# Kernel optimization log

Hardware: AMD Instinct MI355X
Metric: run time of the kernel (lower is better)

## Reference

```python
import jax, jax.numpy as jnp
import numpy as np

D = 512      # units / model dim
H = 8        # num_heads
K = 512      # key_dim (= units in this module)
B = 8
T = 512      # decoder length
S = 512      # encoder length
EPS = 1e-3   # Keras LayerNormalization default epsilon


def _layernorm(x, g, b):
    mu = jnp.mean(x, axis=-1, keepdims=True)
    var = jnp.mean(jnp.square(x - mu), axis=-1, keepdims=True)
    return (x - mu) * jax.lax.rsqrt(var + EPS) * g + b


def _mha(q_in, kv_in, wq, bq, wk, bk, wv, bv, wo, bo, causal):
    # q_in: [B,Tq,D], kv_in: [B,Tk,D]; wq/wk/wv: [D,H,K]; wo: [H,K,D]
    q = jnp.einsum('btd,dhk->bthk', q_in, wq) + bq
    k = jnp.einsum('bsd,dhk->bshk', kv_in, wk) + bk
    v = jnp.einsum('bsd,dhk->bshk', kv_in, wv) + bv
    scores = jnp.einsum('bqhk,bshk->bhqs', q, k) / jnp.sqrt(jnp.float32(K))
    if causal:
        Tq, Tk = q.shape[1], k.shape[1]
        mask = jnp.tril(jnp.ones((Tq, Tk), dtype=bool))
        scores = jnp.where(mask[None, None], scores, jnp.finfo(scores.dtype).min)
    attn = jax.nn.softmax(scores, axis=-1)
    out = jnp.einsum('bhqs,bshk->bqhk', attn, v)
    return jnp.einsum('bqhk,hkd->bqd', out, wo) + bo


def setup_inputs() -> dict:
    key = jax.random.key(0)
    ks = jax.random.split(key, 32)
    sc = 0.02
    d = {
        'in_seq': jax.random.normal(ks[0], (B, S, D), jnp.float32),
        'out_seq': jax.random.normal(ks[1], (B, T, D), jnp.float32),
    }
    i = 2
    for pfx in ('sa', 'ca'):
        d[pfx + '_wq'] = jax.random.normal(ks[i], (D, H, K)) * sc; i += 1
        d[pfx + '_bq'] = jnp.zeros((H, K))
        d[pfx + '_wk'] = jax.random.normal(ks[i], (D, H, K)) * sc; i += 1
        d[pfx + '_bk'] = jnp.zeros((H, K))
        d[pfx + '_wv'] = jax.random.normal(ks[i], (D, H, K)) * sc; i += 1
        d[pfx + '_bv'] = jnp.zeros((H, K))
        d[pfx + '_wo'] = jax.random.normal(ks[i], (H, K, D)) * sc; i += 1
        d[pfx + '_bo'] = jnp.zeros((D,))
        d[pfx + '_lng'] = jnp.ones((D,))
        d[pfx + '_lnb'] = jnp.zeros((D,))
    d['ff_w1'] = jax.random.normal(ks[i], (D, 2 * D)) * sc; i += 1
    d['ff_b1'] = jnp.zeros((2 * D,))
    d['ff_w2'] = jax.random.normal(ks[i], (2 * D, D)) * sc; i += 1
    d['ff_b2'] = jnp.zeros((D,))
    d['ff_lng'] = jnp.ones((D,))
    d['ff_lnb'] = jnp.zeros((D,))
    return d


def reference(in_seq, out_seq,
              sa_wq, sa_bq, sa_wk, sa_bk, sa_wv, sa_bv, sa_wo, sa_bo, sa_lng, sa_lnb,
              ca_wq, ca_bq, ca_wk, ca_bk, ca_wv, ca_bv, ca_wo, ca_bo, ca_lng, ca_lnb,
              ff_w1, ff_b1, ff_w2, ff_b2, ff_lng, ff_lnb):
    # causal self-attention + add + LN
    x = out_seq
    a = _mha(x, x, sa_wq, sa_bq, sa_wk, sa_bk, sa_wv, sa_bv, sa_wo, sa_bo, causal=True)
    x = _layernorm(x + a, sa_lng, sa_lnb)
    # cross-attention + add + LN
    a = _mha(x, in_seq, ca_wq, ca_bq, ca_wk, ca_bk, ca_wv, ca_bv, ca_wo, ca_bo, causal=False)
    x = _layernorm(x + a, ca_lng, ca_lnb)
    # FFN: Dense(2D, gelu) -> Dense(D) (dropout inactive at inference) + add + LN
    h = jax.nn.gelu(x @ ff_w1 + ff_b1, approximate=False)
    x = _layernorm(x + (h @ ff_w2 + ff_b2), ff_lng, ff_lnb)
    return x
```

## Files before the change

### kernel.cpp

```cpp
#include <hip/hip_runtime.h>
#include <math.h>

#define DEV __device__ __forceinline__

typedef __bf16 bf16x8 __attribute__((ext_vector_type(8)));
typedef float f32x4 __attribute__((ext_vector_type(4)));
typedef unsigned short u16x8 __attribute__((ext_vector_type(8)));

typedef const __attribute__((address_space(1))) void gv_t;
typedef __attribute__((address_space(3))) void lv_t;

DEV unsigned short f2bf(float f){
  unsigned int u = __float_as_uint(f);
  u += 0x7fffu + ((u >> 16) & 1u);
  return (unsigned short)(u >> 16);
}
DEV float bf2f(unsigned short u){ return __uint_as_float((unsigned)u << 16); }

DEV void gload16(const void* g, void* l){
  __builtin_amdgcn_global_load_lds((gv_t*)g, (lv_t*)l, 16, 0, 0);
}

DEV void xcd_decode(int& bx, int& by, int& bz){
  const int gx = gridDim.x, gy = gridDim.y;
  const int nwg = gx * gy * gridDim.z;
  int lin = blockIdx.x + gx*(blockIdx.y + gy*blockIdx.z);
  if ((nwg & 7) == 0) lin = (lin & 7)*(nwg >> 3) + (lin >> 3);
  bx = lin % gx; const int t = lin / gx;
  by = t % gy;  bz = t / gy;
}

struct Proj3 {
  const unsigned short* A[3];
  const unsigned short* B[3];
  unsigned short*       C[3];
  const float*          bias[3];
};

__global__ __launch_bounds__(512, 2)
void qkv256(Proj3 pr)
{
  __shared__ unsigned short Ab[2][2][8192];
  __shared__ unsigned short Bb[2][2][8192];

  int bxi, byi, bzi; xcd_decode(bxi, byi, bzi);
  const int m0 = byi*256, n0 = bxi*256;
  const unsigned short* A = pr.A[bzi];
  const unsigned short* B = pr.B[bzi];
  unsigned short*       C = pr.C[bzi];
  const float*       bias = pr.bias[bzi];

  const int tid = threadIdx.x, lane = tid & 63, w = tid >> 6;
  const int wr = w >> 2, wc = w & 3;
  const int l15 = lane & 15, l4 = lane >> 4;

  const int r8  = tid >> 3;
  const int sc8 = ((tid & 7) ^ (r8 & 7)) * 8;

  auto stageA = [&](int buf, int half, int kt){
    #pragma unroll
    for (int j = 0; j < 2; j++){
      const int lr = j*64 + r8;
      gload16(A + (size_t)(m0 + half*128 + lr)*512 + kt + sc8,
              &Ab[buf][half][j*4096 + tid*8]);
    }
  };
  auto stageB = [&](int buf, int half, int kt){
    #pragma unroll
    for (int j = 0; j < 2; j++){
      const int lr = j*64 + r8;
      gload16(B + (size_t)(n0 + half*128 + lr)*512 + kt + sc8,
              &Bb[buf][half][j*4096 + tid*8]);
    }
  };

  f32x4 acc[8][4] = {};

  stageB(0,0,0); stageB(0,1,0);
  stageA(0,0,0); stageA(0,1,0);
  stageA(1,0,64); stageA(1,1,64);
  stageB(1,0,64); stageB(1,1,64);
  asm volatile("s_waitcnt vmcnt(8)" ::: "memory");
  __builtin_amdgcn_s_barrier();
  __builtin_amdgcn_sched_barrier(0);

  const int nt = 8;
  for (int Q = 0; Q < nt; Q++){
    const int cur = Q & 1;
    if (Q > 0){
      if (Q + 1 < nt) asm volatile("s_waitcnt vmcnt(4)" ::: "memory");
      else            asm volatile("s_waitcnt vmcnt(0)" ::: "memory");
      __builtin_amdgcn_s_barrier();
      __builtin_amdgcn_sched_barrier(0);
    }
    bf16x8 bfr[4][2];
    #pragma unroll
    for (int s = 0; s < 4; s++){
      if (s == 0){
        #pragma unroll
        for (int fc = 0; fc < 4; fc++){
          const int R = wc*64 + fc*16 + l15;
          const int hb = R >> 7, lr = R & 127;
          #pragma unroll
          for (int kc = 0; kc < 2; kc++){
            const int cc = (kc*32 + l4*8) ^ ((lr & 7) * 8);
            bfr[fc][kc] = *(const bf16x8*)&Bb[cur][hb][lr*64 + cc];
          }
        }
      }
      bf16x8 ar[2][2];
      #pragma unroll
      for (int f = 0; f < 2; f++){
        const int lr = (s*2 + f)*16 + l15;
        #pragma unroll
        for (int kc = 0; kc < 2; kc++){
          const int cc = (kc*32 + l4*8) ^ ((lr & 7) * 8);
          ar[f][kc] = *(const bf16x8*)&Ab[cur][wr][lr*64 + cc];
        }
      }
      if (s == 0 && Q >= 1 && Q + 1 < nt) stageA(cur ^ 1, 0, (Q+1)*64);
      if (s == 1 && Q >= 1 && Q + 1 < nt) stageA(cur ^ 1, 1, (Q+1)*64);
      if (s == 2 && Q + 2 < nt)           stageB(cur,     0, (Q+2)*64);
      if (s == 3 && Q + 2 < nt)           stageB(cur,     1, (Q+2)*64);

      asm volatile("s_waitcnt lgkmcnt(0)" ::: "memory");
      __builtin_amdgcn_sched_barrier(0);
      __builtin_amdgcn_s_setprio(1);
      #pragma unroll
      for (int f = 0; f < 2; f++)
        #pragma unroll
        for (int fc = 0; fc < 4; fc++)
          #pragma unroll
          for (int kc = 0; kc < 2; kc++)
            acc[s*2+f][fc] = __builtin_amdgcn_mfma_f32_16x16x32_bf16(
                ar[f][kc], bfr[fc][kc], acc[s*2+f][fc], 0, 0, 0);
      __builtin_amdgcn_s_setprio(0);
      __builtin_amdgcn_s_barrier();
      __builtin_amdgcn_sched_barrier(0);
    }
  }

  #pragma unroll
  for (int fr = 0; fr < 8; fr++){
    const int mb = m0 + wr*128 + fr*16 + l4*4;
    #pragma unroll
    for (int fc = 0; fc < 4; fc++){
      const int n = n0 + wc*64 + fc*16 + l15;
      const float bv = bias[n];
      #pragma unroll
      for (int r = 0; r < 4; r++)
        C[(size_t)(mb + r)*4096 + n] = f2bf(acc[fr][fc][r] + bv);
    }
  }
}

template<int CMODE, int CSK>
__global__ __launch_bounds__(512, 2)
void gemm256(const unsigned short* __restrict__ A, const unsigned short* __restrict__ B,
             void* __restrict__ C, const float* __restrict__ bias,
             int M, int N, int K, int lda, int ldb, int ldc,
             size_t aOffH, size_t aOffB, size_t bOffH, size_t bOffB,
             size_t cOffH, size_t cOffB)
{
  __shared__ unsigned short Ab[2][2][8192];
  __shared__ unsigned short Bb[2][2][8192];

  int bxi, byi, bzi; xcd_decode(bxi, byi, bzi);
  const int m0 = byi*256, n0 = bxi*256;
  if (CSK == 1 && n0 > m0 + 255) return;

  const int z = bzi, bb = z >> 3, hh = z & 7;
  A += (size_t)bb*aOffB + (size_t)hh*aOffH;
  B += (size_t)bb*bOffB + (size_t)hh*bOffH;
  const size_t coff = (size_t)bb*cOffB + (size_t)hh*cOffH;

  const int tid = threadIdx.x, lane = tid & 63, w = tid >> 6;
  const int wr = w >> 2, wc = w & 3;
  const int l15 = lane & 15, l4 = lane >> 4;

  int Keff = K;
  if (CSK == 2) Keff = (m0 + 256 < K) ? (m0 + 256) : K;
  const int nt = Keff >> 6;

  const int r8  = tid >> 3;
  const int sc8 = ((tid & 7) ^ (r8 & 7)) * 8;

  auto stageA = [&](int buf, int half, int kt){
    #pragma unroll
    for (int j = 0; j < 2; j++){
      const int lr = j*64 + r8;
      gload16(A + (size_t)(m0 + half*128 + lr)*lda + kt + sc8,
              &Ab[buf][half][j*4096 + tid*8]);
    }
  };
  auto stageB = [&](int buf, int half, int kt){
    #pragma unroll
    for (int j = 0; j < 2; j++){
      const int lr = j*64 + r8;
      gload16(B + (size_t)(n0 + half*128 + lr)*ldb + kt + sc8,
              &Bb[buf][half][j*4096 + tid*8]);
    }
  };

  f32x4 acc[8][4] = {};

  stageB(0,0,0); stageB(0,1,0);
  stageA(0,0,0); stageA(0,1,0);
  if (nt > 1){
    stageA(1,0,64); stageA(1,1,64);
    stageB(1,0,64); stageB(1,1,64);
    asm volatile("s_waitcnt vmcnt(8)" ::: "memory");
  } else {
    asm volatile("s_waitcnt vmcnt(0)" ::: "memory");
  }
  __builtin_amdgcn_s_barrier();
  __builtin_amdgcn_sched_barrier(0);

  for (int Q = 0; Q < nt; Q++){
    const int cur = Q & 1;
    if (Q > 0){
      if (Q + 1 < nt) asm volatile("s_waitcnt vmcnt(4)" ::: "memory");
      else            asm volatile("s_waitcnt vmcnt(0)" ::: "memory");
      __builtin_amdgcn_s_barrier();
      __builtin_amdgcn_sched_barrier(0);
    }
    bf16x8 bfr[4][2];
    #pragma unroll
    for (int s = 0; s < 4; s++){
      if (s == 0){
        #pragma unroll
        for (int fc = 0; fc < 4; fc++){
          const int R = wc*64 + fc*16 + l15;
          const int hb = R >> 7, lr = R & 127;
          #pragma unroll
          for (int kc = 0; kc < 2; kc++){
            const int cc = (kc*32 + l4*8) ^ ((lr & 7) * 8);
            bfr[fc][kc] = *(const bf16x8*)&Bb[cur][hb][lr*64 + cc];
          }
        }
      }
      bf16x8 ar[2][2];
      #pragma unroll
      for (int f = 0; f < 2; f++){
        const int lr = (s*2 + f)*16 + l15;
        #pragma unroll
        for (int kc = 0; kc < 2; kc++){
          const int cc = (kc*32 + l4*8) ^ ((lr & 7) * 8);
          ar[f][kc] = *(const bf16x8*)&Ab[cur][wr][lr*64 + cc];
        }
      }
      if (s == 0 && Q >= 1 && Q + 1 < nt) stageA(cur ^ 1, 0, (Q+1)*64);
      if (s == 1 && Q >= 1 && Q + 1 < nt) stageA(cur ^ 1, 1, (Q+1)*64);
      if (s == 2 && Q + 2 < nt)           stageB(cur,     0, (Q+2)*64);
      if (s == 3 && Q + 2 < nt)           stageB(cur,     1, (Q+2)*64);

      asm volatile("s_waitcnt lgkmcnt(0)" ::: "memory");
      __builtin_amdgcn_sched_barrier(0);
      __builtin_amdgcn_s_setprio(1);
      #pragma unroll
      for (int f = 0; f < 2; f++)
        #pragma unroll
        for (int fc = 0; fc < 4; fc++)
          #pragma unroll
          for (int kc = 0; kc < 2; kc++)
            acc[s*2+f][fc] = __builtin_amdgcn_mfma_f32_16x16x32_bf16(
                ar[f][kc], bfr[fc][kc], acc[s*2+f][fc], 0, 0, 0);
      __builtin_amdgcn_s_setprio(0);
      __builtin_amdgcn_s_barrier();
      __builtin_amdgcn_sched_barrier(0);
    }
  }

  #pragma unroll
  for (int fr = 0; fr < 8; fr++){
    const int mb = m0 + wr*128 + fr*16 + l4*4;
    #pragma unroll
    for (int fc = 0; fc < 4; fc++){
      const int n = n0 + wc*64 + fc*16 + l15;
      const float bv = bias ? bias[n] : 0.0f;
      #pragma unroll
      for (int r = 0; r < 4; r++){
        const float v = acc[fr][fc][r] + bv;
        if (CMODE == 0) ((float*)C)[coff + (size_t)(mb + r)*ldc + n] = v;
        else            ((unsigned short*)C)[coff + (size_t)(mb + r)*ldc + n] = f2bf(v);
      }
    }
  }
}

template<int CMODE>
__global__ __launch_bounds__(256, 2)
void gemm_bt(const unsigned short* __restrict__ A, const unsigned short* __restrict__ B,
             void* __restrict__ C, const float* __restrict__ bias,
             int M, int N, int K, int lda, int ldb, int ldc)
{
  __shared__ unsigned short Ab[2][8192];
  __shared__ unsigned short Bb[2][8192];

  int bxi, byi, bzi; xcd_decode(bxi, byi, bzi);
  (void)bzi;
  const int m0 = byi*128, n0 = bxi*128;

  const int tid = threadIdx.x, lane = tid & 63, w = tid >> 6;
  const int wr = w >> 1, wc = w & 1;
  const int l15 = lane & 15, l4 = lane >> 4;
  const int nt = K >> 6;

  const int r8  = tid >> 3;
  const int sc8 = ((tid & 7) ^ (r8 & 7)) * 8;

  auto stage = [&](int buf, int kt){
    #pragma unroll
    for (int j = 0; j < 4; j++){
      gload16(A + (size_t)(m0 + j*32 + r8)*lda + kt + sc8, &Ab[buf][j*2048 + tid*8]);
      gload16(B + (size_t)(n0 + j*32 + r8)*ldb + kt + sc8, &Bb[buf][j*2048 + tid*8]);
    }
  };

  f32x4 acc[4][4] = {};

  stage(0, 0);
  __syncthreads();
  for (int t = 0; t < nt; t++){
    const int cur = t & 1;
    if (t + 1 < nt) stage(cur ^ 1, (t+1)*64);

    bf16x8 af[4][2], bfr[4][2];
    #pragma unroll
    for (int i = 0; i < 4; i++){
      const int Ra = wr*64 + i*16 + l15;
      const int Rb = wc*64 + i*16 + l15;
      #pragma unroll
      for (int kc = 0; kc < 2; kc++){
        const int ca = (kc*32 + l4*8) ^ ((Ra & 7) * 8);
        const int cb = (kc*32 + l4*8) ^ ((Rb & 7) * 8);
        af[i][kc]  = *(const bf16x8*)&Ab[cur][Ra*64 + ca];
        bfr[i][kc] = *(const bf16x8*)&Bb[cur][Rb*64 + cb];
      }
    }
    #pragma unroll
    for (int i = 0; i < 4; i++)
      #pragma unroll
      for (int jj = 0; jj < 4; jj++)
        #pragma unroll
        for (int kc = 0; kc < 2; kc++)
          acc[i][jj] = __builtin_amdgcn_mfma_f32_16x16x32_bf16(
              af[i][kc], bfr[jj][kc], acc[i][jj], 0, 0, 0);
    __syncthreads();
  }

  #pragma unroll
  for (int i = 0; i < 4; i++){
    const int mbase = m0 + wr*64 + i*16 + l4*4;
    #pragma unroll
    for (int jj = 0; jj < 4; jj++){
      const int n = n0 + wc*64 + jj*16 + l15;
      const float bv = bias ? bias[n] : 0.0f;
      #pragma unroll
      for (int r = 0; r < 4; r++){
        const int m = mbase + r;
        float v = acc[i][jj][r] + bv;
        if (CMODE == 0){
          ((float*)C)[(size_t)m*ldc + n] = v;
        } else if (CMODE == 1){
          ((unsigned short*)C)[(size_t)m*ldc + n] = f2bf(v);
        } else {
          v = 0.5f * v * (1.0f + erff(v * 0.70710678118654752f));
          ((unsigned short*)C)[(size_t)m*ldc + n] = f2bf(v);
        }
      }
    }
  }
}

template<int CAUSAL>
__global__ __launch_bounds__(256)
void softmax_rows(float* __restrict__ scores)
{
  const int row  = blockIdx.x*4 + (threadIdx.x >> 6);
  const int lane = threadIdx.x & 63;
  const int q = row & 511;
  const float* srow = scores + (size_t)row*512;
  float s[8]; float m = -1e30f;
  #pragma unroll
  for (int i = 0; i < 8; i++){
    const int col = lane*8 + i;
    float v = srow[col] * 0.044194173824159216f;
    if (CAUSAL && col > q) v = -1e30f;
    s[i] = v; m = fmaxf(m, v);
  }
  #pragma unroll
  for (int o = 32; o; o >>= 1) m = fmaxf(m, __shfl_xor(m, o));
  float p[8], sum = 0.f;
  #pragma unroll
  for (int i = 0; i < 8; i++){
    float e = __expf(s[i] - m);
    if (CAUSAL && (lane*8 + i) > q) e = 0.f;
    p[i] = e; sum += e;
  }
  #pragma unroll
  for (int o = 32; o; o >>= 1) sum += __shfl_xor(sum, o);
  const float inv = 1.0f / sum;
  unsigned short* prow = (unsigned short*)scores + (size_t)row*1024;
  #pragma unroll
  for (int i = 0; i < 8; i++) prow[lane*8 + i] = f2bf(p[i] * inv);
}

template<int WRITE_BF, int ND, int BFP>
__global__ __launch_bounds__(256)
void ln_rows(const float* __restrict__ x, const void* __restrict__ dbase,
             size_t dstride, const float* __restrict__ bias,
             const float* __restrict__ g, const float* __restrict__ bta,
             float* __restrict__ xo, unsigned short* __restrict__ xb)
{
  const int row = blockIdx.x*4 + (threadIdx.x >> 6);
  const int lane = threadIdx.x & 63;
  const float* xr = x + (size_t)row*512;
  float v[8];
  #pragma unroll
  for (int i = 0; i < 8; i++){
    const int c = lane*8 + i;
    v[i] = xr[c] + (bias ? bias[c] : 0.0f);
  }
  #pragma unroll
  for (int p = 0; p < ND; p++){
    if (BFP){
      const unsigned short* db = (const unsigned short*)dbase;
      u16x8 dv = *(const u16x8*)(db + p*dstride + (size_t)row*512 + lane*8);
      #pragma unroll
      for (int i = 0; i < 8; i++) v[i] += bf2f(dv[i]);
    } else {
      const float* db = (const float*)dbase;
      #pragma unroll
      for (int i = 0; i < 8; i++) v[i] += db[p*dstride + (size_t)row*512 + lane*8 + i];
    }
  }
  float sum = 0.f;
  #pragma unroll
  for (int i = 0; i < 8; i++) sum += v[i];
  #pragma unroll
  for (int o = 32; o; o >>= 1) sum += __shfl_xor(sum, o);
  const float mean = sum * (1.0f/512.0f);
  float s2 = 0.f;
  #pragma unroll
  for (int i = 0; i < 8; i++){ const float t = v[i] - mean; s2 += t*t; }
  #pragma unroll
  for (int o = 32; o; o >>= 1) s2 += __shfl_xor(s2, o);
  const float inv = rsqrtf(s2 * (1.0f/512.0f) + 1e-3f);
  #pragma unroll
  for (int i = 0; i < 8; i++){
    const int c = lane*8 + i;
    const float y = (v[i] - mean)*inv*g[c] + bta[c];
    xo[(size_t)row*512 + c] = y;
    if (WRITE_BF) xb[(size_t)row*512 + c] = f2bf(y);
  }
}

struct Cast2 { const float* s[2]; unsigned short* d[2]; };

__global__ __launch_bounds__(256)
void cast_bf16_k2(Cast2 a, int n)
{
  const int z = blockIdx.y;
  const int i = (blockIdx.x*256 + threadIdx.x)*4;
  if (i < n){
    const float4 v = *(const float4*)(a.s[z] + i);
    uint2 o;
    o.x = (unsigned)f2bf(v.x) | ((unsigned)f2bf(v.y) << 16);
    o.y = (unsigned)f2bf(v.z) | ((unsigned)f2bf(v.w) << 16);
    *(uint2*)(a.d[z] + i) = o;
  }
}

struct TC8 { const float* s[8]; unsigned short* d[8]; };

__global__ __launch_bounds__(256)
void transpose_cast8(TC8 a, int R, int C)
{
  __shared__ float tile[32][33];
  const int z = blockIdx.z;
  const float* src = a.s[z];
  unsigned short* dst = a.d[z];
  const int bx = blockIdx.x*32, by = blockIdx.y*32;
  const int tx = threadIdx.x & 31, ty = threadIdx.x >> 5;
  #pragma unroll
  for (int i = 0; i < 32; i += 8) tile[ty + i][tx] = src[(size_t)(by + ty + i)*C + bx + tx];
  __syncthreads();
  #pragma unroll
  for (int i = 0; i < 32; i += 8) dst[(size_t)(bx + ty + i)*R + by + tx] = f2bf(tile[tx][ty + i]);
}

__global__ __launch_bounds__(256)
void transpose_v(const unsigned short* __restrict__ src, unsigned short* __restrict__ dst)
{
  __shared__ unsigned short t[32][34];
  const int z = blockIdx.z, b = z >> 3, h = z & 7;
  const int s0 = blockIdx.y*32, k0 = blockIdx.x*32;
  const int tx = threadIdx.x & 31, ty4 = (threadIdx.x >> 5) * 4;
  #pragma unroll
  for (int i = 0; i < 4; i++)
    t[ty4 + i][tx] = src[(size_t)(b*512 + s0 + ty4 + i)*4096 + h*512 + k0 + tx];
  __syncthreads();
  unsigned short* d = dst + ((size_t)z*512 + k0)*512 + s0;
  #pragma unroll
  for (int i = 0; i < 4; i++)
    d[(size_t)(ty4 + i)*512 + tx] = t[tx][ty4 + i];
}

extern "C" void kernel_launch(void* const* d_in, const int* in_sizes, int n_in,
                              void* d_out, int out_size, void* d_ws, size_t ws_size,
                              hipStream_t stream)
{
  (void)in_sizes; (void)n_in; (void)out_size; (void)ws_size;

  const float* in_seq  = (const float*)d_in[0];
  const float* out_seq = (const float*)d_in[1];
  const float* sa_wq = (const float*)d_in[2];  const float* sa_bq = (const float*)d_in[3];
  const float* sa_wk = (const float*)d_in[4];  const float* sa_bk = (const float*)d_in[5];
  const float* sa_wv = (const float*)d_in[6];  const float* sa_bv = (const float*)d_in[7];
  const float* sa_wo = (const float*)d_in[8];  const float* sa_bo = (const float*)d_in[9];
  const float* sa_lng = (const float*)d_in[10]; const float* sa_lnb = (const float*)d_in[11];
  const float* ca_wq = (const float*)d_in[12]; const float* ca_bq = (const float*)d_in[13];
  const float* ca_wk = (const float*)d_in[14]; const float* ca_bk = (const float*)d_in[15];
  const float* ca_wv = (const float*)d_in[16]; const float* ca_bv = (const float*)d_in[17];
  const float* ca_wo = (const float*)d_in[18]; const float* ca_bo = (const float*)d_in[19];
  const float* ca_lng = (const float*)d_in[20]; const float* ca_lnb = (const float*)d_in[21];
  const float* ff_w1 = (const float*)d_in[22]; const float* ff_b1 = (const float*)d_in[23];
  const float* ff_w2 = (const float*)d_in[24]; const float* ff_b2 = (const float*)d_in[25];
  const float* ff_lng = (const float*)d_in[26]; const float* ff_lnb = (const float*)d_in[27];

  char* ws = (char*)d_ws;
  size_t off = 0;
  auto alloc = [&](size_t bytes){ char* p = ws + off; off += (bytes + 255) & ~(size_t)255; return p; };

  unsigned short* wT[8];
  for (int i = 0; i < 8; i++) wT[i] = (unsigned short*)alloc(4096ULL*512*2);
  unsigned short* w1T  = (unsigned short*)alloc(1024ULL*512*2);
  unsigned short* w2T  = (unsigned short*)alloc(512ULL*1024*2);
  unsigned short* xbf  = (unsigned short*)alloc(4096ULL*512*2);
  unsigned short* inbf = (unsigned short*)alloc(4096ULL*512*2);
  unsigned short* qb   = (unsigned short*)alloc(4096ULL*4096*2);
  unsigned short* kb   = (unsigned short*)alloc(4096ULL*4096*2);
  unsigned short* vT   = (unsigned short*)alloc(64ULL*512*512*2);
  float*          sc   = (float*)alloc(64ULL*512*512*4);
  float*          xcur = (float*)alloc(4096ULL*512*4);

  unsigned short* vb   = (unsigned short*)sc;
  unsigned short* part = (unsigned short*)sc;
  const size_t PART_STRIDE = 2097152;

  Cast2 c2{{out_seq, in_seq}, {xbf, inbf}};
  cast_bf16_k2<<<dim3(2048,2), 256, 0, stream>>>(c2, 4096*512);

  TC8 tqkv{{sa_wq, sa_wk, sa_wv, ca_wq, ca_wk, ca_wv, nullptr, nullptr},
           {wT[0], wT[1], wT[2], wT[4], wT[5], wT[6], nullptr, nullptr}};
  transpose_cast8<<<dim3(128,16,6), 256, 0, stream>>>(tqkv, 512, 4096);
  TC8 two{{sa_wo, ca_wo, nullptr,nullptr,nullptr,nullptr,nullptr,nullptr},
          {wT[3], wT[7], nullptr,nullptr,nullptr,nullptr,nullptr,nullptr}};
  transpose_cast8<<<dim3(16,128,2), 256, 0, stream>>>(two, 4096, 512);
  TC8 tw1{{ff_w1, nullptr,nullptr,nullptr,nullptr,nullptr,nullptr,nullptr},
          {w1T, nullptr,nullptr,nullptr,nullptr,nullptr,nullptr,nullptr}};
  transpose_cast8<<<dim3(32,16,1), 256, 0, stream>>>(tw1, 512, 1024);
  TC8 tw2{{ff_w2, nullptr,nullptr,nullptr,nullptr,nullptr,nullptr,nullptr},
          {w2T, nullptr,nullptr,nullptr,nullptr,nullptr,nullptr,nullptr}};
  transpose_cast8<<<dim3(16,32,1), 256, 0, stream>>>(tw2, 1024, 512);

  #define G256(MODE, CSK, Apt, Bpt, Cpt, BIAS, M, N, K, LDA, LDB, LDC, Z, aH, aB, bH, bB, cH, cB) \
    gemm256<MODE, CSK><<<dim3((N)/256,(M)/256,(Z)), 512, 0, stream>>>( \
      (const unsigned short*)(Apt), (const unsigned short*)(Bpt), (void*)(Cpt), BIAS, \
      M, N, K, LDA, LDB, LDC, aH, aB, bH, bB, cH, cB)

  Proj3 saP{{xbf, xbf, xbf}, {wT[0], wT[1], wT[2]}, {qb, kb, vb}, {sa_bq, sa_bk, sa_bv}};
  qkv256<<<dim3(16,16,3), 512, 0, stream>>>(saP);
  transpose_v<<<dim3(16,16,64), 256, 0, stream>>>(vb, vT);
  G256(0, 1, qb, kb, sc, nullptr, 512, 512, 512, 4096, 4096, 512, 64,
       512, 2097152, 512, 2097152, 262144, 2097152);
  softmax_rows<1><<<8192, 256, 0, stream>>>(sc);
  G256(1, 2, sc, vT, kb, nullptr, 512, 512, 512, 1024, 512, 4096, 64,
       524288, 4194304, 262144, 2097152, 512, 2097152);
  G256(1, 0, kb, wT[3], part, nullptr, 4096, 512, 512, 4096, 4096, 512, 8,
       512, 0, 512, 0, PART_STRIDE, 0);
  ln_rows<1, 8, 1><<<1024, 256, 0, stream>>>(out_seq, part, PART_STRIDE,
                                             sa_bo, sa_lng, sa_lnb, xcur, xbf);

  Proj3 caP{{xbf, inbf, inbf}, {wT[4], wT[5], wT[6]}, {qb, kb, vb}, {ca_bq, ca_bk, ca_bv}};
  qkv256<<<dim3(16,16,3), 512, 0, stream>>>(caP);
  transpose_v<<<dim3(16,16,64), 256, 0, stream>>>(vb, vT);
  G256(0, 0, qb, kb, sc, nullptr, 512, 512, 512, 4096, 4096, 512, 64,
       512, 2097152, 512, 2097152, 262144, 2097152);
  softmax_rows<0><<<8192, 256, 0, stream>>>(sc);
  G256(1, 0, sc, vT, kb, nullptr, 512, 512, 512, 1024, 512, 4096, 64,
       524288, 4194304, 262144, 2097152, 512, 2097152);
  G256(1, 0, kb, wT[7], part, nullptr, 4096, 512, 512, 4096, 4096, 512, 8,
       512, 0, 512, 0, PART_STRIDE, 0);
  ln_rows<1, 8, 1><<<1024, 256, 0, stream>>>(xcur, part, PART_STRIDE,
                                             ca_bo, ca_lng, ca_lnb, xcur, xbf);

  gemm_bt<2><<<dim3(8,32,1), 256, 0, stream>>>(
      xbf, w1T, (void*)qb, ff_b1, 4096, 1024, 512, 512, 512, 1024);
  G256(1, 0, qb, w2T, part, nullptr, 4096, 512, 128, 1024, 1024, 512, 8,
       128, 0, 128, 0, PART_STRIDE, 0);
  ln_rows<0, 8, 1><<<1024, 256, 0, stream>>>(xcur, part, PART_STRIDE,
                                             ff_b2, ff_lng, ff_lnb, (float*)d_out, nullptr);

  #undef G256
}
```

Measured before the change: 490.0 us.

## Fuse V transpose into QKV epilogue and store attention scores in bf16

The QKV projection kernel now writes V directly in transposed per-head layout, staging it through LDS in its epilogue, so the separate transpose_v launches go away. The QK^T score GEMM now writes bf16 instead of fp32, and softmax reads and writes bf16 in place with vectorized 16-byte accesses. This cuts score-buffer traffic roughly in half and removes two kernels. The trade-offs are reduced precision of the pre-softmax logits and extra LDS round-trips with syncs in the V epilogue.

```diff
diff --git a/kernel.cpp b/kernel.cpp
--- a/kernel.cpp
+++ b/kernel.cpp
@@ -140,16 +140,60 @@
     }
   }
 
-  #pragma unroll
-  for (int fr = 0; fr < 8; fr++){
-    const int mb = m0 + wr*128 + fr*16 + l4*4;
-    #pragma unroll
-    for (int fc = 0; fc < 4; fc++){
-      const int n = n0 + wc*64 + fc*16 + l15;
-      const float bv = bias[n];
-      #pragma unroll
-      for (int r = 0; r < 4; r++)
-        C[(size_t)(mb + r)*4096 + n] = f2bf(acc[fr][fc][r] + bv);
+  if (bzi != 2){
+    #pragma unroll
+    for (int fr = 0; fr < 8; fr++){
+      const int mb = m0 + wr*128 + fr*16 + l4*4;
+      #pragma unroll
+      for (int fc = 0; fc < 4; fc++){
+        const int n = n0 + wc*64 + fc*16 + l15;
+        const float bv = bias[n];
+        #pragma unroll
+        for (int r = 0; r < 4; r++)
+          C[(size_t)(mb + r)*4096 + n] = f2bf(acc[fr][fc][r] + bv);
+      }
+    }
+  } else {
+    const int zz = (m0 >> 9)*8 + (n0 >> 9);
+    const int s_base  = m0 & 511;
+    const int ko_base = n0 & 511;
+    unsigned short* lds = (unsigned short*)Ab;
+    const int PADW = 140;
+    #pragma unroll 1
+    for (int mh = 0; mh < 2; mh++){
+      #pragma unroll 1
+      for (int nh = 0; nh < 2; nh++){
+        __syncthreads();
+        if (wr == mh && (wc >> 1) == nh){
+          #pragma unroll
+          for (int fr = 0; fr < 8; fr++)
+            #pragma unroll
+            for (int fc = 0; fc < 4; fc++){
+              const int n  = n0 + wc*64 + fc*16 + l15;
+              const float bv = bias[n];
+              const int nl = (wc & 1)*64 + fc*16 + l15;
+              #pragma unroll
+              for (int r = 0; r < 4; r++){
+                const int ml = fr*16 + l4*4 + r;
+                lds[ml*PADW + nl] = f2bf(acc[fr][fc][r] + bv);
+              }
+            }
+        }
+        __syncthreads();
+        const int kol = tid >> 2, s0c = (tid & 3)*32;
+        unsigned short* dst = C + (size_t)zz*262144
+                              + (size_t)(ko_base + nh*128 + kol)*512
+                              + s_base + mh*128 + s0c;
+        u16x8 vbuf[4];
+        #pragma unroll
+        for (int g = 0; g < 4; g++)
+          #pragma unroll
+          for (int j = 0; j < 8; j++)
+            vbuf[g][j] = lds[(s0c + g*8 + j)*PADW + kol];
+        #pragma unroll
+        for (int g = 0; g < 4; g++)
+          *(u16x8*)(dst + g*8) = vbuf[g];
+      }
     }
   }
 }
@@ -375,17 +419,18 @@
 
 template<int CAUSAL>
 __global__ __launch_bounds__(256)
-void softmax_rows(float* __restrict__ scores)
+void softmax_rows(unsigned short* __restrict__ scores)
 {
   const int row  = blockIdx.x*4 + (threadIdx.x >> 6);
   const int lane = threadIdx.x & 63;
   const int q = row & 511;
-  const float* srow = scores + (size_t)row*512;
+  unsigned short* srow = scores + (size_t)row*512;
+  u16x8 sv = *(const u16x8*)(srow + lane*8);
   float s[8]; float m = -1e30f;
   #pragma unroll
   for (int i = 0; i < 8; i++){
     const int col = lane*8 + i;
-    float v = srow[col] * 0.044194173824159216f;
+    float v = bf2f(sv[i]) * 0.044194173824159216f;
     if (CAUSAL && col > q) v = -1e30f;
     s[i] = v; m = fmaxf(m, v);
   }
@@ -401,9 +446,10 @@
   #pragma unroll
   for (int o = 32; o; o >>= 1) sum += __shfl_xor(sum, o);
   const float inv = 1.0f / sum;
-  unsigned short* prow = (unsigned short*)scores + (size_t)row*1024;
-  #pragma unroll
-  for (int i = 0; i < 8; i++) prow[lane*8 + i] = f2bf(p[i] * inv);
+  u16x8 pv;
+  #pragma unroll
+  for (int i = 0; i < 8; i++) pv[i] = f2bf(p[i] * inv);
+  *(u16x8*)(srow + lane*8) = pv;
 }
 
 template<int WRITE_BF, int ND, int BFP>
@@ -488,23 +534,6 @@
   __syncthreads();
   #pragma unroll
   for (int i = 0; i < 32; i += 8) dst[(size_t)(bx + ty + i)*R + by + tx] = f2bf(tile[tx][ty + i]);
-}
-
-__global__ __launch_bounds__(256)
-void transpose_v(const unsigned short* __restrict__ src, unsigned short* __restrict__ dst)
-{
-  __shared__ unsigned short t[32][34];
-  const int z = blockIdx.z, b = z >> 3, h = z & 7;
-  const int s0 = blockIdx.y*32, k0 = blockIdx.x*32;
-  const int tx = threadIdx.x & 31, ty4 = (threadIdx.x >> 5) * 4;
-  #pragma unroll
-  for (int i = 0; i < 4; i++)
-    t[ty4 + i][tx] = src[(size_t)(b*512 + s0 + ty4 + i)*4096 + h*512 + k0 + tx];
-  __syncthreads();
-  unsigned short* d = dst + ((size_t)z*512 + k0)*512 + s0;
-  #pragma unroll
-  for (int i = 0; i < 4; i++)
-    d[(size_t)(ty4 + i)*512 + tx] = t[tx][ty4 + i];
 }
 
 extern "C" void kernel_launch(void* const* d_in, const int* in_sizes, int n_in,
@@ -542,11 +571,10 @@
   unsigned short* qb   = (unsigned short*)alloc(4096ULL*4096*2);
   unsigned short* kb   = (unsigned short*)alloc(4096ULL*4096*2);
   unsigned short* vT   = (unsigned short*)alloc(64ULL*512*512*2);
-  float*          sc   = (float*)alloc(64ULL*512*512*4);
+  unsigned short* scb  = (unsigned short*)alloc(64ULL*512*512*2);
   float*          xcur = (float*)alloc(4096ULL*512*4);
 
-  unsigned short* vb   = (unsigned short*)sc;
-  unsigned short* part = (unsigned short*)sc;
+  unsigned short* part = scb;
   const size_t PART_STRIDE = 2097152;
 
   Cast2 c2{{out_seq, in_seq}, {xbf, inbf}};
@@ -570,27 +598,25 @@
       (const unsigned short*)(Apt), (const unsigned short*)(Bpt), (void*)(Cpt), BIAS, \
       M, N, K, LDA, LDB, LDC, aH, aB, bH, bB, cH, cB)
 
-  Proj3 saP{{xbf, xbf, xbf}, {wT[0], wT[1], wT[2]}, {qb, kb, vb}, {sa_bq, sa_bk, sa_bv}};
+  Proj3 saP{{xbf, xbf, xbf}, {wT[0], wT[1], wT[2]}, {qb, kb, vT}, {sa_bq, sa_bk, sa_bv}};
   qkv256<<<dim3(16,16,3), 512, 0, stream>>>(saP);
-  transpose_v<<<dim3(16,16,64), 256, 0, stream>>>(vb, vT);
-  G256(0, 1, qb, kb, sc, nullptr, 512, 512, 512, 4096, 4096, 512, 64,
+  G256(1, 1, qb, kb, scb, nullptr, 512, 512, 512, 4096, 4096, 512, 64,
        512, 2097152, 512, 2097152, 262144, 2097152);
-  softmax_rows<1><<<8192, 256, 0, stream>>>(sc);
-  G256(1, 2, sc, vT, kb, nullptr, 512, 512, 512, 1024, 512, 4096, 64,
-       524288, 4194304, 262144, 2097152, 512, 2097152);
+  softmax_rows<1><<<8192, 256, 0, stream>>>(scb);
+  G256(1, 2, scb, vT, kb, nullptr, 512, 512, 512, 512, 512, 4096, 64,
+       262144, 2097152, 262144, 2097152, 512, 2097152);
   G256(1, 0, kb, wT[3], part, nullptr, 4096, 512, 512, 4096, 4096, 512, 8,
        512, 0, 512, 0, PART_STRIDE, 0);
   ln_rows<1, 8, 1><<<1024, 256, 0, stream>>>(out_seq, part, PART_STRIDE,
                                              sa_bo, sa_lng, sa_lnb, xcur, xbf);
 
-  Proj3 caP{{xbf, inbf, inbf}, {wT[4], wT[5], wT[6]}, {qb, kb, vb}, {ca_bq, ca_bk, ca_bv}};
+  Proj3 caP{{xbf, inbf, inbf}, {wT[4], wT[5], wT[6]}, {qb, kb, vT}, {ca_bq, ca_bk, ca_bv}};
   qkv256<<<dim3(16,16,3), 512, 0, stream>>>(caP);
-  transpose_v<<<dim3(16,16,64), 256, 0, stream>>>(vb, vT);
-  G256(0, 0, qb, kb, sc, nullptr, 512, 512, 512, 4096, 4096, 512, 64,
+  G256(1, 0, qb, kb, scb, nullptr, 512, 512, 512, 4096, 4096, 512, 64,
        512, 2097152, 512, 2097152, 262144, 2097152);
-  softmax_rows<0><<<8192, 256, 0, stream>>>(sc);
-  G256(1, 0, sc, vT, kb, nullptr, 512, 512, 512, 1024, 512, 4096, 64,
-       524288, 4194304, 262144, 2097152, 512, 2097152);
+  softmax_rows<0><<<8192, 256, 0, stream>>>(scb);
+  G256(1, 0, scb, vT, kb, nullptr, 512, 512, 512, 512, 512, 4096, 64,
+       262144, 2097152, 262144, 2097152, 512, 2097152);
   G256(1, 0, kb, wT[7], part, nullptr, 4096, 512, 512, 4096, 4096, 512, 8,
        512, 0, 512, 0, PART_STRIDE, 0);
   ln_rows<1, 8, 1><<<1024, 256, 0, stream>>>(xcur, part, PART_STRIDE,
```

Measured after the change: 493.5 us. Within noise of the previous version (+0.7%).
